# Optimization experiments

Hardware: AMD Instinct MI355X
Metric: run time of the kernel (lower is better)

The kernel has to match this reference:

```python
import jax, jax.numpy as jnp
import numpy as np

EPS = 1e-05
DILATION = 1

def setup_inputs() -> dict:
    key = jax.random.key(0)
    k1, k2 = jax.random.split(key)
    B, T, D, K = 4, 4096, 2048, 4
    x = jax.random.normal(k1, (B, T, D), dtype=jnp.float32)
    norm_weight = jnp.ones((D,), dtype=jnp.float32)
    conv_weight = jax.random.normal(k2, (D, 1, K), dtype=jnp.float32) * (1.0 / np.sqrt(K))
    return {"x": x, "norm_weight": norm_weight, "conv_weight": conv_weight}

def reference(x, norm_weight, conv_weight):
    B, T, D = x.shape
    K = conv_weight.shape[-1]
    pad = (K - 1) * DILATION
    # RMSNorm over last dim
    ms = jnp.mean(jnp.square(x), axis=-1, keepdims=True)
    y = x * jax.lax.rsqrt(ms + EPS) * norm_weight
    # to channel-first [B, D, T]
    y = jnp.transpose(y, (0, 2, 1))
    # causal depthwise conv: left-pad (K-1)*dilation, valid conv == torch pad-both + slice[:T]
    y = jax.lax.conv_general_dilated(
        y, conv_weight,
        window_strides=(1,),
        padding=[(pad, 0)],
        rhs_dilation=(DILATION,),
        dimension_numbers=("NCH", "OIH", "NCH"),
        feature_group_count=D,
    )
    # SiLU then back to [B, T, D]
    y = y * jax.nn.sigmoid(y)
    return jnp.transpose(y, (0, 2, 1))
```

## Files before the change

### kernel.cpp

```cpp
#include <hip/hip_runtime.h>
#include <math.h>

#define D_DIM 2048
#define T_DIM 4096
#define TT    16
#define NT    (D_DIM / 4)
#define NW    (NT / 64)

typedef float vfloat4 __attribute__((ext_vector_type(4)));

__device__ __forceinline__ float row_partial(float4 v) {
    float p = v.x * v.x + v.y * v.y + v.z * v.z + v.w * v.w;
#pragma unroll
    for (int off = 32; off > 0; off >>= 1) p += __shfl_down(p, off, 64);
    return p;
}

__device__ __forceinline__ float inv_from(const float* sp) {
    float4 a = *(const float4*)sp;
    float4 b = *(const float4*)(sp + 4);
    float s = a.x + a.y + a.z + a.w + b.x + b.y + b.z + b.w;
    return rsqrtf(s * (1.0f / D_DIM) + 1e-5f);
}

__device__ __forceinline__ float silu(float v) {
    return v * __builtin_amdgcn_rcpf(1.f + __expf(-v));
}

__device__ __forceinline__ void nt_store4(float* p, float a, float b, float c, float d) {
    vfloat4 v = { a, b, c, d };
    __builtin_nontemporal_store(v, (vfloat4*)p);
}

__global__ __launch_bounds__(NT, 4) void fused_kernel(
    const float* __restrict__ x,
    const float* __restrict__ g,
    const float* __restrict__ w,
    float* __restrict__ out)
{
    const int b    = blockIdx.y;
    const int t0   = blockIdx.x * TT;
    const int tid  = threadIdx.x;
    const int d0   = tid * 4;
    const int lane = tid & 63;
    const int wid  = tid >> 6;

    __shared__ __align__(16) float hpart[3][NW];
    __shared__ __align__(16) float part[2][2][NW];

    const float* xb = x   + (size_t)b * T_DIM * D_DIM + d0;
    float*       ob = out + (size_t)b * T_DIM * D_DIM + d0;

    float4 hv[3];
#pragma unroll
    for (int r = 0; r < 3; ++r) {
        const int t = t0 - 3 + r;
        hv[r] = (t >= 0) ? *(const float4*)(xb + (size_t)t * D_DIM)
                         : make_float4(0.f, 0.f, 0.f, 0.f);
    }
    float4 cur0 = *(const float4*)(xb + (size_t)(t0 + 0) * D_DIM);
    float4 cur1 = *(const float4*)(xb + (size_t)(t0 + 1) * D_DIM);
    float4 nxt0 = *(const float4*)(xb + (size_t)(t0 + 2) * D_DIM);
    float4 nxt1 = *(const float4*)(xb + (size_t)(t0 + 3) * D_DIM);

    const float4 gv = *(const float4*)(g + d0);
    float wgt[4][4];
#pragma unroll
    for (int j = 0; j < 4; ++j) {
        float4 wv = *(const float4*)(w + (size_t)(d0 + j) * 4);
        wgt[j][0] = wv.x; wgt[j][1] = wv.y; wgt[j][2] = wv.z; wgt[j][3] = wv.w;
    }

#pragma unroll
    for (int r = 0; r < 3; ++r) {
        float p = row_partial(hv[r]);
        if (lane == 0) hpart[r][wid] = p;
    }
    __syncthreads();

    float win[3][4];
#pragma unroll
    for (int r = 0; r < 3; ++r) {
        const float inv = inv_from(hpart[r]);
        win[r][0] = hv[r].x * inv * gv.x;
        win[r][1] = hv[r].y * inv * gv.y;
        win[r][2] = hv[r].z * inv * gv.z;
        win[r][3] = hv[r].w * inv * gv.w;
    }

#pragma unroll
    for (int i = 0; i < TT; i += 2) {
        const int slot = (i >> 1) & 1;
        float p0 = row_partial(cur0);
        float p1 = row_partial(cur1);
        if (lane == 0) { part[slot][0][wid] = p0; part[slot][1][wid] = p1; }
        __syncthreads();

        float4 f0, f1;
        if (i + 4 < TT) {
            f0 = *(const float4*)(xb + (size_t)(t0 + i + 4) * D_DIM);
            f1 = *(const float4*)(xb + (size_t)(t0 + i + 5) * D_DIM);
        } else {
            f0 = make_float4(0.f, 0.f, 0.f, 0.f);
            f1 = f0;
        }

        const float r0 = inv_from(part[slot][0]);
        const float r1 = inv_from(part[slot][1]);
        const float y0[4] = { cur0.x * r0 * gv.x, cur0.y * r0 * gv.y,
                              cur0.z * r0 * gv.z, cur0.w * r0 * gv.w };
        const float y1[4] = { cur1.x * r1 * gv.x, cur1.y * r1 * gv.y,
                              cur1.z * r1 * gv.z, cur1.w * r1 * gv.w };

        float o0[4], o1[4];
#pragma unroll
        for (int j = 0; j < 4; ++j) {
            const float v0 = wgt[j][0] * win[0][j] + wgt[j][1] * win[1][j] +
                             wgt[j][2] * win[2][j] + wgt[j][3] * y0[j];
            o0[j] = silu(v0);
            const float v1 = wgt[j][0] * win[1][j] + wgt[j][1] * win[2][j] +
                             wgt[j][2] * y0[j]     + wgt[j][3] * y1[j];
            o1[j] = silu(v1);
        }
        nt_store4(ob + (size_t)(t0 + i)     * D_DIM, o0[0], o0[1], o0[2], o0[3]);
        nt_store4(ob + (size_t)(t0 + i + 1) * D_DIM, o1[0], o1[1], o1[2], o1[3]);

#pragma unroll
        for (int j = 0; j < 4; ++j) {
            win[0][j] = win[2][j];
            win[1][j] = y0[j];
            win[2][j] = y1[j];
        }
        cur0 = nxt0; cur1 = nxt1; nxt0 = f0; nxt1 = f1;
    }
}

extern "C" void kernel_launch(void* const* d_in, const int* in_sizes, int n_in,
                              void* d_out, int out_size, void* d_ws, size_t ws_size,
                              hipStream_t stream) {
    const float* x = (const float*)d_in[0];
    const float* g = (const float*)d_in[1];
    const float* w = (const float*)d_in[2];
    float* out = (float*)d_out;

    const int total = in_sizes[0];
    const int rows  = total / D_DIM;
    const int B     = rows / T_DIM;

    dim3 grid(T_DIM / TT, B);
    fused_kernel<<<grid, NT, 0, stream>>>(x, g, w, out);
}
```

Measured before the change: 239.3 us.

## Load whole time tile upfront and reduce all row norms with one barrier

```diff
diff --git a/kernel.cpp b/kernel.cpp
--- a/kernel.cpp
+++ b/kernel.cpp
@@ -45,8 +45,7 @@
     const int lane = tid & 63;
     const int wid  = tid >> 6;
 
-    __shared__ __align__(16) float hpart[3][NW];
-    __shared__ __align__(16) float part[2][2][NW];
+    __shared__ __align__(16) float part[TT + 3][NW];
 
     const float* xb = x   + (size_t)b * T_DIM * D_DIM + d0;
     float*       ob = out + (size_t)b * T_DIM * D_DIM + d0;
@@ -58,10 +57,10 @@
         hv[r] = (t >= 0) ? *(const float4*)(xb + (size_t)t * D_DIM)
                          : make_float4(0.f, 0.f, 0.f, 0.f);
     }
-    float4 cur0 = *(const float4*)(xb + (size_t)(t0 + 0) * D_DIM);
-    float4 cur1 = *(const float4*)(xb + (size_t)(t0 + 1) * D_DIM);
-    float4 nxt0 = *(const float4*)(xb + (size_t)(t0 + 2) * D_DIM);
-    float4 nxt1 = *(const float4*)(xb + (size_t)(t0 + 3) * D_DIM);
+    float4 xv[TT];
+#pragma unroll
+    for (int i = 0; i < TT; ++i)
+        xv[i] = *(const float4*)(xb + (size_t)(t0 + i) * D_DIM);
 
     const float4 gv = *(const float4*)(g + d0);
     float wgt[4][4];
@@ -74,14 +73,19 @@
 #pragma unroll
     for (int r = 0; r < 3; ++r) {
         float p = row_partial(hv[r]);
-        if (lane == 0) hpart[r][wid] = p;
+        if (lane == 0) part[r][wid] = p;
+    }
+#pragma unroll
+    for (int i = 0; i < TT; ++i) {
+        float p = row_partial(xv[i]);
+        if (lane == 0) part[3 + i][wid] = p;
     }
     __syncthreads();
 
     float win[3][4];
 #pragma unroll
     for (int r = 0; r < 3; ++r) {
-        const float inv = inv_from(hpart[r]);
+        const float inv = inv_from(part[r]);
         win[r][0] = hv[r].x * inv * gv.x;
         win[r][1] = hv[r].y * inv * gv.y;
         win[r][2] = hv[r].z * inv * gv.z;
@@ -89,49 +93,25 @@
     }
 
 #pragma unroll
-    for (int i = 0; i < TT; i += 2) {
-        const int slot = (i >> 1) & 1;
-        float p0 = row_partial(cur0);
-        float p1 = row_partial(cur1);
-        if (lane == 0) { part[slot][0][wid] = p0; part[slot][1][wid] = p1; }
-        __syncthreads();
-
-        float4 f0, f1;
-        if (i + 4 < TT) {
-            f0 = *(const float4*)(xb + (size_t)(t0 + i + 4) * D_DIM);
-            f1 = *(const float4*)(xb + (size_t)(t0 + i + 5) * D_DIM);
-        } else {
-            f0 = make_float4(0.f, 0.f, 0.f, 0.f);
-            f1 = f0;
-        }
-
-        const float r0 = inv_from(part[slot][0]);
-        const float r1 = inv_from(part[slot][1]);
-        const float y0[4] = { cur0.x * r0 * gv.x, cur0.y * r0 * gv.y,
-                              cur0.z * r0 * gv.z, cur0.w * r0 * gv.w };
-        const float y1[4] = { cur1.x * r1 * gv.x, cur1.y * r1 * gv.y,
-                              cur1.z * r1 * gv.z, cur1.w * r1 * gv.w };
-
-        float o0[4], o1[4];
+    for (int i = 0; i < TT; ++i) {
+        const float inv = inv_from(part[3 + i]);
+        const float y0[4] = { xv[i].x * inv * gv.x, xv[i].y * inv * gv.y,
+                              xv[i].z * inv * gv.z, xv[i].w * inv * gv.w };
+        float o0[4];
 #pragma unroll
         for (int j = 0; j < 4; ++j) {
-            const float v0 = wgt[j][0] * win[0][j] + wgt[j][1] * win[1][j] +
-                             wgt[j][2] * win[2][j] + wgt[j][3] * y0[j];
-            o0[j] = silu(v0);
-            const float v1 = wgt[j][0] * win[1][j] + wgt[j][1] * win[2][j] +
-                             wgt[j][2] * y0[j]     + wgt[j][3] * y1[j];
-            o1[j] = silu(v1);
+            const float v = wgt[j][0] * win[0][j] + wgt[j][1] * win[1][j] +
+                            wgt[j][2] * win[2][j] + wgt[j][3] * y0[j];
+            o0[j] = silu(v);
         }
-        nt_store4(ob + (size_t)(t0 + i)     * D_DIM, o0[0], o0[1], o0[2], o0[3]);
-        nt_store4(ob + (size_t)(t0 + i + 1) * D_DIM, o1[0], o1[1], o1[2], o1[3]);
+        nt_store4(ob + (size_t)(t0 + i) * D_DIM, o0[0], o0[1], o0[2], o0[3]);
 
 #pragma unroll
         for (int j = 0; j < 4; ++j) {
-            win[0][j] = win[2][j];
-            win[1][j] = y0[j];
-            win[2][j] = y1[j];
+            win[0][j] = win[1][j];
+            win[1][j] = win[2][j];
+            win[2][j] = y0[j];
         }
-        cur0 = nxt0; cur1 = nxt1; nxt0 = f0; nxt1 = f1;
     }
 }
 
```

Measured after the change: 238.6 us. No clear change (-0.3%).
